# Performance work log

Measured on AMD Instinct MI355X. Metric: run time of the kernel, lower is better.

The kernel has to match this reference:

```python
import jax, jax.numpy as jnp
import numpy as np

D_K = 256

def setup_inputs() -> dict:
    key = jax.random.key(0)
    k1, k2, k3, k4 = jax.random.split(key, 4)
    B, S, D = 4, 4096, 256
    x = jax.random.normal(k1, (B, S, D), dtype=jnp.float32)
    scale = 1.0 / np.sqrt(D)
    W_q = jax.random.normal(k2, (D, D_K), dtype=jnp.float32) * scale
    W_k = jax.random.normal(k3, (D, D_K), dtype=jnp.float32) * scale
    W_v = jax.random.normal(k4, (D, D_K), dtype=jnp.float32) * scale
    return {"x": x, "W_q": W_q, "W_k": W_k, "W_v": W_v}

def reference(x, W_q, W_k, W_v):
    # x: [B, S, D]; weights: [D, d_k]
    B, S, D = x.shape
    Q = jnp.einsum('bsd,dk->bsk', x, W_q)
    K = jnp.einsum('bsd,dk->bsk', x, W_k)
    V = jnp.einsum('bsd,dk->bsk', x, W_v)
    scores = jnp.einsum('bqk,bsk->bqs', Q, K) / jnp.sqrt(jnp.float32(D_K))  # [B, S, S]
    causal = jnp.tril(jnp.ones((S, S), dtype=bool))
    scores = jnp.where(causal[None, :, :], scores, -jnp.inf)
    weights = jax.nn.softmax(scores, axis=-1)
    return jnp.einsum('bqs,bsk->bqk', weights, V)
```

## Files before the change

### kernel.cpp

```cpp
#include <hip/hip_runtime.h>
#include <hip/hip_bf16.h>
#include <cstdint>


typedef __bf16 b8v __attribute__((ext_vector_type(8)));
typedef __bf16 b4v __attribute__((ext_vector_type(4)));
typedef float  f4v __attribute__((ext_vector_type(4)));
typedef float  f16v __attribute__((ext_vector_type(16)));
typedef int    i4v __attribute__((ext_vector_type(4)));
typedef int    i2v __attribute__((ext_vector_type(2)));

#define MFMA16(a, b, c) __builtin_amdgcn_mfma_f32_16x16x32_bf16((a), (b), (c), 0, 0, 0)
#define MFMA32(a, b, c) __builtin_amdgcn_mfma_f32_32x32x16_bf16((a), (b), (c), 0, 0, 0)

#define GLOAD_LDS(gsrc, ldst)                                                        \
  __builtin_amdgcn_global_load_lds((const __attribute__((address_space(1))) void*)(gsrc), \
                                   (__attribute__((address_space(3))) void*)(ldst), 16, 0, 0)

#define SCALE_Q 0.09016844005f
#define MASKVAL -3.0e38f
#define M0VAL   -1.0e30f

static constexpr int UT = 4224;
static constexpr size_t WS_WT = 0;
static constexpr size_t WS_Q  = 524288;
static constexpr size_t WS_K  = WS_Q + 8388608;
static constexpr size_t WS_VT = WS_K + 8388608;
static constexpr size_t WS_PART = WS_VT + 8388608;

__global__ void prep_wt(const float* __restrict__ Wq, const float* __restrict__ Wk,
                        const float* __restrict__ Wv, __bf16* __restrict__ wt) {
  int gid = blockIdx.x * blockDim.x + threadIdx.x;
  int w = gid >> 16, rem = gid & 65535;
  int c = rem >> 8, d = rem & 255;
  const float* W = (w == 0) ? Wq : (w == 1) ? Wk : Wv;
  float v = W[d * 256 + c];
  if (w == 0) v *= SCALE_Q;
  wt[gid] = (__bf16)v;
}

__global__ void __launch_bounds__(256, 2) proj_qkv(
    const float* __restrict__ x, const __bf16* __restrict__ wt,
    __bf16* __restrict__ Qw, __bf16* __restrict__ Kw, __bf16* __restrict__ Vt) {
  __shared__ __bf16 w_lds[64][264];
  __shared__ __bf16 v_lds[64][72];
  const int tid = threadIdx.x;
  const int wv = tid >> 6, lane = tid & 63, c = lane & 15, g = lane >> 4;
  const int ww = blockIdx.x >> 8, rb = blockIdx.x & 255;
  const int rowbase = rb * 64;
  const int batch = rb >> 6, sblk = rb & 63;

  b8v xf[8];
  {
    const float* xr = x + (size_t)(rowbase + wv * 16 + c) * 256;
#pragma unroll
    for (int ks = 0; ks < 8; ++ks) {
      const float4 a0 = *reinterpret_cast<const float4*>(xr + 32 * ks + 8 * g);
      const float4 a1 = *reinterpret_cast<const float4*>(xr + 32 * ks + 8 * g + 4);
      b8v f;
      f[0] = (__bf16)a0.x; f[1] = (__bf16)a0.y; f[2] = (__bf16)a0.z; f[3] = (__bf16)a0.w;
      f[4] = (__bf16)a1.x; f[5] = (__bf16)a1.y; f[6] = (__bf16)a1.z; f[7] = (__bf16)a1.w;
      xf[ks] = f;
    }
  }
  const int srow = tid >> 2, sch = tid & 3;
  for (int ct = 0; ct < 4; ++ct) {
    __syncthreads();
    {
      const i4v* src = reinterpret_cast<const i4v*>(
          wt + ((size_t)(ww * 256 + ct * 64 + srow)) * 256 + sch * 64);
      i4v* dst = reinterpret_cast<i4v*>(&w_lds[srow][sch * 64]);
#pragma unroll
      for (int j = 0; j < 8; ++j) dst[j] = src[j];
    }
    __syncthreads();
    f4v pacc[4];
#pragma unroll
    for (int i = 0; i < 4; ++i) pacc[i] = (f4v){0.f, 0.f, 0.f, 0.f};
#pragma unroll
    for (int ks = 0; ks < 8; ++ks) {
#pragma unroll
      for (int nf = 0; nf < 4; ++nf) {
        b8v wf = *reinterpret_cast<const b8v*>(&w_lds[16 * nf + c][32 * ks + 8 * g]);
        pacc[nf] = MFMA16(xf[ks], wf, pacc[nf]);
      }
    }
    if (ww < 2) {
      __bf16* o = (ww == 0) ? Qw : Kw;
      const int row0 = rowbase + wv * 16 + 4 * g;
#pragma unroll
      for (int nf = 0; nf < 4; ++nf) {
        const int col = ct * 64 + 16 * nf + c;
#pragma unroll
        for (int r = 0; r < 4; ++r)
          o[(size_t)(row0 + r) * 256 + col] = (__bf16)pacc[nf][r];
      }
    } else {
      const int sp = 16 * wv + 4 * g;
#pragma unroll
      for (int nf = 0; nf < 4; ++nf) {
        b4v pk;
        pk[0] = (__bf16)pacc[nf][0]; pk[1] = (__bf16)pacc[nf][1];
        pk[2] = (__bf16)pacc[nf][2]; pk[3] = (__bf16)pacc[nf][3];
        *reinterpret_cast<b4v*>(&v_lds[16 * nf + c][sp]) = pk;
      }
      __syncthreads();
      {
        const int dd = tid >> 2, ch = tid & 3;
        const b8v* sp8 = reinterpret_cast<const b8v*>(&v_lds[dd][ch * 16]);
        __bf16* dst =
            Vt + ((size_t)(batch * 256 + ct * 64 + dd)) * 4096 + sblk * 64 + ch * 16;
        reinterpret_cast<b8v*>(dst)[0] = sp8[0];
        reinterpret_cast<b8v*>(dst)[1] = sp8[1];
      }
    }
  }
}

__global__ void __launch_bounds__(256, 2) attn_fwd(
    const __bf16* __restrict__ Qw, const __bf16* __restrict__ Kw,
    const __bf16* __restrict__ Vt, float* __restrict__ out,
    __bf16* __restrict__ part, float* __restrict__ ml, int NB) {
  extern __shared__ char smem[];
  float* bc = reinterpret_cast<float*>(smem + 65536);

  const int tid = threadIdx.x;
  const int wv = tid >> 6, lane = tid & 63;
  const int q5 = lane & 31, hi = lane >> 5;

  const int p = blockIdx.x, xcd = p & 7;
  const int lb = (xcd >> 1) * (NB >> 2) + (xcd & 1) * (NB >> 3) + (p >> 3);

  int u = (int)(((long long)lb * UT) / NB);
  const int u1 = (int)(((long long)(lb + 1) * UT) / NB);

  while (u < u1) {
    const int bb = u / 1056;
    const int r0 = u - bb * 1056;
    int q = 0;
    while ((q + 1) * (q + 2) <= r0) ++q;
    const int g0 = bb * 1056 + q * (q + 1);
    const int len = 2 * q + 2;
    const int ge = g0 + len;
    const int re = (u1 < ge) ? u1 : ge;
    const int ta = u - g0, tb = re - g0;
    const bool direct = (ta == 0) && (tb == len);

    const __bf16* Kg = Kw + (size_t)bb * 4096 * 256;
    const __bf16* Vg = Vt + (size_t)bb * 256 * 4096;

    auto stage = [&](int s, int tt) {
      char* Kd = smem + s * 32768;
      char* Vd = Kd + 16384;
#pragma unroll
      for (int i = 0; i < 4; ++i) {
        const int n = i * 256 + tid;
        const int r = n >> 5, cp = n & 31;
        const __bf16* src = Kg + (size_t)(tt * 32 + r) * 256 + ((cp ^ r) << 3);
        GLOAD_LDS(src, Kd + ((i * 256 + wv * 64) << 4));
      }
#pragma unroll
      for (int i = 0; i < 4; ++i) {
        const int n = i * 256 + tid;
        const int d = n >> 2, cp = n & 3;
        const __bf16* src =
            Vg + (size_t)d * 4096 + tt * 32 + ((cp ^ ((d >> 3) & 3)) << 3);
        GLOAD_LDS(src, Vd + ((i * 256 + wv * 64) << 4));
      }
    };

    b8v qf[16];
    {
      const __bf16* qr =
          Qw + ((size_t)(bb * 4096 + q * 128 + wv * 32 + q5)) * 256 + 8 * hi;
#pragma unroll
      for (int ks = 0; ks < 16; ++ks)
        qf[ks] = *reinterpret_cast<const b8v*>(qr + ks * 16);
    }

    f16v acc[8];
#pragma unroll
    for (int i = 0; i < 8; ++i)
#pragma unroll
      for (int j = 0; j < 16; ++j) acc[i][j] = 0.f;
    float m = M0VAL, lsum = 0.f;
    const int qg = q * 128 + wv * 32 + q5;
    const int ttEnd = 2 * tb;

    stage(0, 2 * ta);
    __syncthreads();

    for (int tt = 2 * ta; tt < ttEnd; ++tt) {
      const int cur = tt & 1;
      if (tt + 1 < ttEnd) stage(cur ^ 1, tt + 1);

      f16v s;
#pragma unroll
      for (int j = 0; j < 16; ++j) s[j] = 0.f;
      const char* kb0 = smem + cur * 32768 + q5 * 512;
      __builtin_amdgcn_s_setprio(1);
#pragma unroll
      for (int ks = 0; ks < 16; ++ks) {
        const int co = (((ks << 1) | hi) ^ q5) << 4;
        const b8v k0 = *reinterpret_cast<const b8v*>(kb0 + co);
        s = MFMA32(k0, qf[ks], s);
      }
      __builtin_amdgcn_s_setprio(0);

      if (tt * 32 + 31 > q * 128 + wv * 32) {
#pragma unroll
        for (int reg = 0; reg < 16; ++reg) {
          const int R = (reg & 3) + 8 * (reg >> 2) + 4 * hi;
          if (tt * 32 + R > qg) s[reg] = MASKVAL;
        }
      }
      float p0 = s[0], p1 = s[1], p2 = s[2], p3 = s[3];
#pragma unroll
      for (int j = 4; j < 16; j += 4) {
        p0 = fmaxf(p0, s[j]); p1 = fmaxf(p1, s[j + 1]);
        p2 = fmaxf(p2, s[j + 2]); p3 = fmaxf(p3, s[j + 3]);
      }
      const float pm = fmaxf(fmaxf(p0, p1), fmaxf(p2, p3));

      if (!__all(pm - m <= 8.0f)) {
        const float pm2 = fmaxf(pm, __shfl_xor(pm, 32));
        const float mnew = fmaxf(m, pm2);
        const float fac = exp2f(m - mnew);
        bc[wv * 32 + q5] = fac;
        lsum *= fac;
        m = mnew;
#pragma unroll
        for (int reg = 0; reg < 16; ++reg) {
          const float fr = bc[wv * 32 + ((reg & 3) + 8 * (reg >> 2) + 4 * hi)];
#pragma unroll
          for (int db = 0; db < 8; ++db) acc[db][reg] *= fr;
        }
      }
#pragma unroll
      for (int j = 0; j < 16; ++j) s[j] = exp2f(s[j] - m);
      {
        float u0 = 0.f, u1s = 0.f, u2 = 0.f, u3 = 0.f;
#pragma unroll
        for (int j = 0; j < 16; j += 4) {
          u0 += s[j]; u1s += s[j + 1]; u2 += s[j + 2]; u3 += s[j + 3];
        }
        lsum += (u0 + u1s) + (u2 + u3);
      }
      unsigned a0[4], a1[4];
#pragma unroll
      for (int mb = 0; mb < 4; ++mb) {
        b4v pk;
        pk[0] = (__bf16)s[4 * mb]; pk[1] = (__bf16)s[4 * mb + 1];
        pk[2] = (__bf16)s[4 * mb + 2]; pk[3] = (__bf16)s[4 * mb + 3];
        const uint2 uu = *reinterpret_cast<uint2*>(&pk);
        a0[mb] = uu.x; a1[mb] = uu.y;
      }
      const char* vbase = smem + cur * 32768 + 16384 + q5 * 64;
#pragma unroll
      for (int ks = 0; ks < 2; ++ks) {
        i4v wi;
#if __has_builtin(__builtin_amdgcn_permlane32_swap)
        const i2v e0 = __builtin_amdgcn_permlane32_swap((int)a0[2 * ks],
                                                        (int)a0[2 * ks + 1], false, false);
        const i2v e1 = __builtin_amdgcn_permlane32_swap((int)a1[2 * ks],
                                                        (int)a1[2 * ks + 1], false, false);
        wi[0] = e0[0]; wi[1] = e1[0]; wi[2] = e0[1]; wi[3] = e1[1];
#else
        const unsigned x0 = (unsigned)__shfl_xor((int)a0[2 * ks], 32);
        const unsigned x1 = (unsigned)__shfl_xor((int)a1[2 * ks], 32);
        const unsigned y0 = (unsigned)__shfl_xor((int)a0[2 * ks + 1], 32);
        const unsigned y1 = (unsigned)__shfl_xor((int)a1[2 * ks + 1], 32);
        wi[0] = hi ? (int)y0 : (int)a0[2 * ks];
        wi[1] = hi ? (int)y1 : (int)a1[2 * ks];
        wi[2] = hi ? (int)a0[2 * ks + 1] : (int)x0;
        wi[3] = hi ? (int)a1[2 * ks + 1] : (int)x1;
#endif
        const b8v pa = *reinterpret_cast<b8v*>(&wi);
        const int cov = ((((ks << 1) | hi)) ^ ((q5 >> 3) & 3)) << 4;
        __builtin_amdgcn_s_setprio(1);
#pragma unroll
        for (int db = 0; db < 8; ++db) {
          const b8v vf =
              *reinterpret_cast<const b8v*>(vbase + db * 2048 + cov);
          acc[db] = MFMA32(pa, vf, acc[db]);
        }
        __builtin_amdgcn_s_setprio(0);
      }
      __syncthreads();
    }

    lsum += __shfl_xor(lsum, 32);
    if (direct) {
      const float inv = 1.f / lsum;
      bc[wv * 32 + q5] = inv;
#pragma unroll
      for (int reg = 0; reg < 16; ++reg) {
        const int R = (reg & 3) + 8 * (reg >> 2) + 4 * hi;
        const float ivr = bc[wv * 32 + R];
        float* orow =
            out + ((size_t)(bb * 4096 + q * 128 + wv * 32 + R)) * 256 + q5;
#pragma unroll
        for (int db = 0; db < 8; ++db) orow[db * 32] = acc[db][reg] * ivr;
      }
    } else {
      const int sidx = bb * 32 + q;
      int base = 0;
      for (int sdx = 0; sdx < sidx; ++sdx) {
        const int sq = sdx & 31, sbb = sdx >> 5;
        const int h0 = sbb * 1056 + sq * (sq + 1);
        const int h1 = h0 + 2 * sq + 2;
        const int k = (h1 * NB + UT - 1) / UT - ((h0 + 1) * NB + UT - 1) / UT;
        if (k > 0) base += k + 1;
      }
      const int idx = ((u + 1) * NB + UT - 1) / UT - ((g0 + 1) * NB + UT - 1) / UT;
      const int slot = base + idx;
      __bf16* pbase = part + (size_t)slot * 32768;
#pragma unroll
      for (int reg = 0; reg < 16; ++reg) {
        const int R = (reg & 3) + 8 * (reg >> 2) + 4 * hi;
        __bf16* prow = pbase + (size_t)(wv * 32 + R) * 256 + q5;
#pragma unroll
        for (int db = 0; db < 8; ++db) prow[db * 32] = (__bf16)acc[db][reg];
      }
      if (hi == 0) {
        float2* ml2 = reinterpret_cast<float2*>(ml);
        ml2[(size_t)slot * 128 + wv * 32 + q5] = make_float2(m, lsum);
      }
    }
    u = re;
  }
}

__global__ void __launch_bounds__(256) combine_k(
    const __bf16* __restrict__ part, const float* __restrict__ ml,
    float* __restrict__ out, int NB) {
  const int sidx = blockIdx.x >> 2, rq = blockIdx.x & 3;
  const int bb = sidx >> 5, q = sidx & 31;
  const int g0 = bb * 1056 + q * (q + 1);
  const int g1 = g0 + 2 * q + 2;
  const int nbi = (g1 * NB + UT - 1) / UT - ((g0 + 1) * NB + UT - 1) / UT;
  if (nbi <= 0) return;
  const int nch = nbi + 1;
  int base = 0;
  for (int s = 0; s < sidx; ++s) {
    const int sq = s & 31, sbb = s >> 5;
    const int h0 = sbb * 1056 + sq * (sq + 1);
    const int h1 = h0 + 2 * sq + 2;
    const int k = (h1 * NB + UT - 1) / UT - ((h0 + 1) * NB + UT - 1) / UT;
    if (k > 0) base += k + 1;
  }
  const int row = rq * 32 + (threadIdx.x >> 3);
  const int c0 = (threadIdx.x & 7) * 32;
  const float2* ml2 = reinterpret_cast<const float2*>(ml);

  float mx = MASKVAL;
  for (int cc = 0; cc < nch; ++cc)
    mx = fmaxf(mx, ml2[(size_t)(base + cc) * 128 + row].x);
  float den = 0.f;
  for (int cc = 0; cc < nch; ++cc) {
    const float2 pr = ml2[(size_t)(base + cc) * 128 + row];
    den += exp2f(pr.x - mx) * pr.y;
  }
  const float inv = 1.f / den;
  f4v o4[8];
#pragma unroll
  for (int i = 0; i < 8; ++i) o4[i] = (f4v){0.f, 0.f, 0.f, 0.f};
  for (int cc = 0; cc < nch; ++cc) {
    const float w = exp2f(ml2[(size_t)(base + cc) * 128 + row].x - mx) * inv;
    const b8v* src = reinterpret_cast<const b8v*>(
        part + ((size_t)(base + cc) * 128 + row) * 256 + c0);
#pragma unroll
    for (int k = 0; k < 4; ++k) {
      const b8v v = src[k];
#pragma unroll
      for (int j = 0; j < 4; ++j) {
        o4[2 * k][j] += w * (float)v[j];
        o4[2 * k + 1][j] += w * (float)v[4 + j];
      }
    }
  }
  float* dst = out + ((size_t)(bb * 4096 + q * 128 + row)) * 256 + c0;
#pragma unroll
  for (int k = 0; k < 8; ++k) reinterpret_cast<f4v*>(dst)[k] = o4[k];
}

extern "C" void kernel_launch(void* const* d_in, const int* in_sizes, int n_in,
                              void* d_out, int out_size, void* d_ws, size_t ws_size,
                              hipStream_t stream) {
  const float* x  = reinterpret_cast<const float*>(d_in[0]);
  const float* Wq = reinterpret_cast<const float*>(d_in[1]);
  const float* Wk = reinterpret_cast<const float*>(d_in[2]);
  const float* Wv = reinterpret_cast<const float*>(d_in[3]);
  char* ws = reinterpret_cast<char*>(d_ws);
  __bf16* wt = reinterpret_cast<__bf16*>(ws + WS_WT);
  __bf16* Qw = reinterpret_cast<__bf16*>(ws + WS_Q);
  __bf16* Kw = reinterpret_cast<__bf16*>(ws + WS_K);
  __bf16* Vt = reinterpret_cast<__bf16*>(ws + WS_VT);
  float* out = reinterpret_cast<float*>(d_out);

  const int cand[5] = {512, 384, 256, 128, 64};
  int NB = 64, slots = 0;
  for (int ci = 0; ci < 5; ++ci) {
    const int nb = cand[ci];
    int sl = 0;
    for (int s = 0; s < 128; ++s) {
      const int sq = s & 31, sbb = s >> 5;
      const int h0 = sbb * 1056 + sq * (sq + 1);
      const int h1 = h0 + 2 * sq + 2;
      const int k = (h1 * nb + UT - 1) / UT - ((h0 + 1) * nb + UT - 1) / UT;
      if (k > 0) sl += k + 1;
    }
    const size_t need = WS_PART + (size_t)sl * 65536 + (size_t)sl * 1024;
    if (ws_size >= need) { NB = nb; slots = sl; break; }
  }
  __bf16* part = reinterpret_cast<__bf16*>(ws + WS_PART);
  float* mlp = reinterpret_cast<float*>(ws + WS_PART + (size_t)slots * 65536);

  prep_wt<<<768, 256, 0, stream>>>(Wq, Wk, Wv, wt);
  proj_qkv<<<768, 256, 0, stream>>>(x, wt, Qw, Kw, Vt);

  constexpr int kSmem = 66048;
  (void)hipFuncSetAttribute(reinterpret_cast<const void*>(attn_fwd),
                            hipFuncAttributeMaxDynamicSharedMemorySize, kSmem);
  attn_fwd<<<NB, 256, kSmem, stream>>>(Qw, Kw, Vt, out, part, mlp, NB);
  combine_k<<<512, 256, 0, stream>>>(part, mlp, out, NB);
}
```

Baseline: 162.6 us.

## Load K/V fragments directly from global memory instead of LDS double-buffering

Removes the LDS staging of K and V tiles (global_load_lds double buffer plus per-tile barriers). Each lane now reads its MFMA operands straight from global memory, relying on L2/L1 caching. The score MFMA chain is split into two independent accumulators to shorten the dependency chain. The LDS broadcasts of rescale factors are replaced with wave shuffles. This frees shared memory and barriers but makes all four waves re-fetch the same K/V data, and the V reads are strided with poor coalescing.

```diff
diff --git a/kernel.cpp b/kernel.cpp
--- a/kernel.cpp
+++ b/kernel.cpp
@@ -12,10 +12,6 @@
 
 #define MFMA16(a, b, c) __builtin_amdgcn_mfma_f32_16x16x32_bf16((a), (b), (c), 0, 0, 0)
 #define MFMA32(a, b, c) __builtin_amdgcn_mfma_f32_32x32x16_bf16((a), (b), (c), 0, 0, 0)
-
-#define GLOAD_LDS(gsrc, ldst)                                                        \
-  __builtin_amdgcn_global_load_lds((const __attribute__((address_space(1))) void*)(gsrc), \
-                                   (__attribute__((address_space(3))) void*)(ldst), 16, 0, 0)
 
 #define SCALE_Q 0.09016844005f
 #define MASKVAL -3.0e38f
@@ -121,9 +117,6 @@
     const __bf16* __restrict__ Qw, const __bf16* __restrict__ Kw,
     const __bf16* __restrict__ Vt, float* __restrict__ out,
     __bf16* __restrict__ part, float* __restrict__ ml, int NB) {
-  extern __shared__ char smem[];
-  float* bc = reinterpret_cast<float*>(smem + 65536);
-
   const int tid = threadIdx.x;
   const int wv = tid >> 6, lane = tid & 63;
   const int q5 = lane & 31, hi = lane >> 5;
@@ -146,28 +139,8 @@
     const int ta = u - g0, tb = re - g0;
     const bool direct = (ta == 0) && (tb == len);
 
-    const __bf16* Kg = Kw + (size_t)bb * 4096 * 256;
-    const __bf16* Vg = Vt + (size_t)bb * 256 * 4096;
-
-    auto stage = [&](int s, int tt) {
-      char* Kd = smem + s * 32768;
-      char* Vd = Kd + 16384;
-#pragma unroll
-      for (int i = 0; i < 4; ++i) {
-        const int n = i * 256 + tid;
-        const int r = n >> 5, cp = n & 31;
-        const __bf16* src = Kg + (size_t)(tt * 32 + r) * 256 + ((cp ^ r) << 3);
-        GLOAD_LDS(src, Kd + ((i * 256 + wv * 64) << 4));
-      }
-#pragma unroll
-      for (int i = 0; i < 4; ++i) {
-        const int n = i * 256 + tid;
-        const int d = n >> 2, cp = n & 3;
-        const __bf16* src =
-            Vg + (size_t)d * 4096 + tt * 32 + ((cp ^ ((d >> 3) & 3)) << 3);
-        GLOAD_LDS(src, Vd + ((i * 256 + wv * 64) << 4));
-      }
-    };
+    const __bf16* Krow = Kw + ((size_t)bb * 4096 + q5) * 256 + 8 * hi;
+    const __bf16* Vrow = Vt + ((size_t)bb * 256 + q5) * 4096 + 8 * hi;
 
     b8v qf[16];
     {
@@ -187,25 +160,21 @@
     const int qg = q * 128 + wv * 32 + q5;
     const int ttEnd = 2 * tb;
 
-    stage(0, 2 * ta);
-    __syncthreads();
-
     for (int tt = 2 * ta; tt < ttEnd; ++tt) {
-      const int cur = tt & 1;
-      if (tt + 1 < ttEnd) stage(cur ^ 1, tt + 1);
-
-      f16v s;
-#pragma unroll
-      for (int j = 0; j < 16; ++j) s[j] = 0.f;
-      const char* kb0 = smem + cur * 32768 + q5 * 512;
+      const __bf16* kbase = Krow + (size_t)tt * 32 * 256;
+      f16v sA, sB;
+#pragma unroll
+      for (int j = 0; j < 16; ++j) { sA[j] = 0.f; sB[j] = 0.f; }
       __builtin_amdgcn_s_setprio(1);
 #pragma unroll
-      for (int ks = 0; ks < 16; ++ks) {
-        const int co = (((ks << 1) | hi) ^ q5) << 4;
-        const b8v k0 = *reinterpret_cast<const b8v*>(kb0 + co);
-        s = MFMA32(k0, qf[ks], s);
+      for (int k8 = 0; k8 < 8; ++k8) {
+        const b8v ka = *reinterpret_cast<const b8v*>(kbase + k8 * 16);
+        const b8v kb = *reinterpret_cast<const b8v*>(kbase + 128 + k8 * 16);
+        sA = MFMA32(ka, qf[k8], sA);
+        sB = MFMA32(kb, qf[8 + k8], sB);
       }
       __builtin_amdgcn_s_setprio(0);
+      f16v s = sA + sB;
 
       if (tt * 32 + 31 > q * 128 + wv * 32) {
 #pragma unroll
@@ -226,12 +195,11 @@
         const float pm2 = fmaxf(pm, __shfl_xor(pm, 32));
         const float mnew = fmaxf(m, pm2);
         const float fac = exp2f(m - mnew);
-        bc[wv * 32 + q5] = fac;
         lsum *= fac;
         m = mnew;
 #pragma unroll
         for (int reg = 0; reg < 16; ++reg) {
-          const float fr = bc[wv * 32 + ((reg & 3) + 8 * (reg >> 2) + 4 * hi)];
+          const float fr = __shfl(fac, (reg & 3) + 8 * (reg >> 2) + 4 * hi);
 #pragma unroll
           for (int db = 0; db < 8; ++db) acc[db][reg] *= fr;
         }
@@ -255,7 +223,7 @@
         const uint2 uu = *reinterpret_cast<uint2*>(&pk);
         a0[mb] = uu.x; a1[mb] = uu.y;
       }
-      const char* vbase = smem + cur * 32768 + 16384 + q5 * 64;
+      const __bf16* vbase = Vrow + tt * 32;
 #pragma unroll
       for (int ks = 0; ks < 2; ++ks) {
         i4v wi;
@@ -276,27 +244,23 @@
         wi[3] = hi ? (int)a1[2 * ks + 1] : (int)x1;
 #endif
         const b8v pa = *reinterpret_cast<b8v*>(&wi);
-        const int cov = ((((ks << 1) | hi)) ^ ((q5 >> 3) & 3)) << 4;
         __builtin_amdgcn_s_setprio(1);
 #pragma unroll
         for (int db = 0; db < 8; ++db) {
-          const b8v vf =
-              *reinterpret_cast<const b8v*>(vbase + db * 2048 + cov);
+          const b8v vf = *reinterpret_cast<const b8v*>(vbase + (size_t)db * 131072 + ks * 16);
           acc[db] = MFMA32(pa, vf, acc[db]);
         }
         __builtin_amdgcn_s_setprio(0);
       }
-      __syncthreads();
     }
 
     lsum += __shfl_xor(lsum, 32);
     if (direct) {
       const float inv = 1.f / lsum;
-      bc[wv * 32 + q5] = inv;
 #pragma unroll
       for (int reg = 0; reg < 16; ++reg) {
         const int R = (reg & 3) + 8 * (reg >> 2) + 4 * hi;
-        const float ivr = bc[wv * 32 + R];
+        const float ivr = __shfl(inv, R);
         float* orow =
             out + ((size_t)(bb * 4096 + q * 128 + wv * 32 + R)) * 256 + q5;
 #pragma unroll
@@ -418,10 +382,6 @@
 
   prep_wt<<<768, 256, 0, stream>>>(Wq, Wk, Wv, wt);
   proj_qkv<<<768, 256, 0, stream>>>(x, wt, Qw, Kw, Vt);
-
-  constexpr int kSmem = 66048;
-  (void)hipFuncSetAttribute(reinterpret_cast<const void*>(attn_fwd),
-                            hipFuncAttributeMaxDynamicSharedMemorySize, kSmem);
-  attn_fwd<<<NB, 256, kSmem, stream>>>(Qw, Kw, Vt, out, part, mlp, NB);
+  attn_fwd<<<NB, 256, 0, stream>>>(Qw, Kw, Vt, out, part, mlp, NB);
   combine_k<<<512, 256, 0, stream>>>(part, mlp, out, NB);
 }
```

Result: slower. 222.7 us (+37.0%).

## Read V directly from global memory and split QK accumulation chains

Applied to the files above, without the earlier changes.

V tiles are no longer staged through LDS. Each lane reads its V fragments straight from global memory (mostly L2-resident), which halves LDS use to let more blocks fit per CU. The QK^T MFMA chain is also split into two independent accumulators to shorten the dependency chain. In exchange, every wave issues uncoalesced-ish global loads for V on the critical path of the PV MFMAs, with no prefetching.

```diff
diff --git a/kernel.cpp b/kernel.cpp
--- a/kernel.cpp
+++ b/kernel.cpp
@@ -122,7 +122,7 @@
     const __bf16* __restrict__ Vt, float* __restrict__ out,
     __bf16* __restrict__ part, float* __restrict__ ml, int NB) {
   extern __shared__ char smem[];
-  float* bc = reinterpret_cast<float*>(smem + 65536);
+  float* bc = reinterpret_cast<float*>(smem + 32768);
 
   const int tid = threadIdx.x;
   const int wv = tid >> 6, lane = tid & 63;
@@ -147,11 +147,10 @@
     const bool direct = (ta == 0) && (tb == len);
 
     const __bf16* Kg = Kw + (size_t)bb * 4096 * 256;
-    const __bf16* Vg = Vt + (size_t)bb * 256 * 4096;
+    const __bf16* Vrow = Vt + ((size_t)bb * 256 + q5) * 4096 + 8 * hi;
 
     auto stage = [&](int s, int tt) {
-      char* Kd = smem + s * 32768;
-      char* Vd = Kd + 16384;
+      char* Kd = smem + s * 16384;
 #pragma unroll
       for (int i = 0; i < 4; ++i) {
         const int n = i * 256 + tid;
@@ -159,14 +158,6 @@
         const __bf16* src = Kg + (size_t)(tt * 32 + r) * 256 + ((cp ^ r) << 3);
         GLOAD_LDS(src, Kd + ((i * 256 + wv * 64) << 4));
       }
-#pragma unroll
-      for (int i = 0; i < 4; ++i) {
-        const int n = i * 256 + tid;
-        const int d = n >> 2, cp = n & 3;
-        const __bf16* src =
-            Vg + (size_t)d * 4096 + tt * 32 + ((cp ^ ((d >> 3) & 3)) << 3);
-        GLOAD_LDS(src, Vd + ((i * 256 + wv * 64) << 4));
-      }
     };
 
     b8v qf[16];
@@ -194,18 +185,22 @@
       const int cur = tt & 1;
       if (tt + 1 < ttEnd) stage(cur ^ 1, tt + 1);
 
-      f16v s;
-#pragma unroll
-      for (int j = 0; j < 16; ++j) s[j] = 0.f;
-      const char* kb0 = smem + cur * 32768 + q5 * 512;
+      f16v sA, sB;
+#pragma unroll
+      for (int j = 0; j < 16; ++j) { sA[j] = 0.f; sB[j] = 0.f; }
+      const char* kb0 = smem + cur * 16384 + q5 * 512;
       __builtin_amdgcn_s_setprio(1);
 #pragma unroll
-      for (int ks = 0; ks < 16; ++ks) {
-        const int co = (((ks << 1) | hi) ^ q5) << 4;
-        const b8v k0 = *reinterpret_cast<const b8v*>(kb0 + co);
-        s = MFMA32(k0, qf[ks], s);
+      for (int k8 = 0; k8 < 8; ++k8) {
+        const int coA = (((k8 << 1) | hi) ^ q5) << 4;
+        const int coB = ((16 + (k8 << 1) | hi) ^ q5) << 4;
+        const b8v ka = *reinterpret_cast<const b8v*>(kb0 + coA);
+        const b8v kb = *reinterpret_cast<const b8v*>(kb0 + coB);
+        sA = MFMA32(ka, qf[k8], sA);
+        sB = MFMA32(kb, qf[8 + k8], sB);
       }
       __builtin_amdgcn_s_setprio(0);
+      f16v s = sA + sB;
 
       if (tt * 32 + 31 > q * 128 + wv * 32) {
 #pragma unroll
@@ -255,7 +250,7 @@
         const uint2 uu = *reinterpret_cast<uint2*>(&pk);
         a0[mb] = uu.x; a1[mb] = uu.y;
       }
-      const char* vbase = smem + cur * 32768 + 16384 + q5 * 64;
+      const __bf16* vbase = Vrow + tt * 32;
 #pragma unroll
       for (int ks = 0; ks < 2; ++ks) {
         i4v wi;
@@ -276,12 +271,11 @@
         wi[3] = hi ? (int)a1[2 * ks + 1] : (int)x1;
 #endif
         const b8v pa = *reinterpret_cast<b8v*>(&wi);
-        const int cov = ((((ks << 1) | hi)) ^ ((q5 >> 3) & 3)) << 4;
         __builtin_amdgcn_s_setprio(1);
 #pragma unroll
         for (int db = 0; db < 8; ++db) {
           const b8v vf =
-              *reinterpret_cast<const b8v*>(vbase + db * 2048 + cov);
+              *reinterpret_cast<const b8v*>(vbase + (size_t)db * 131072 + ks * 16);
           acc[db] = MFMA32(pa, vf, acc[db]);
         }
         __builtin_amdgcn_s_setprio(0);
@@ -419,7 +413,7 @@
   prep_wt<<<768, 256, 0, stream>>>(Wq, Wk, Wv, wt);
   proj_qkv<<<768, 256, 0, stream>>>(x, wt, Qw, Kw, Vt);
 
-  constexpr int kSmem = 66048;
+  constexpr int kSmem = 32768 + 1024;
   (void)hipFuncSetAttribute(reinterpret_cast<const void*>(attn_fwd),
                             hipFuncAttributeMaxDynamicSharedMemorySize, kSmem);
   attn_fwd<<<NB, 256, kSmem, stream>>>(Qw, Kw, Vt, out, part, mlp, NB);
```

Result: slower. 211.7 us (+30.2%).

## Write first split partial directly to output, split QK accumulator chains

Applied to the files above, without the earlier changes.

For split query blocks, the first chunk's unnormalized fp32 accumulator is now written straight into the output buffer, and only later chunks go to the bf16 partial buffer. The combine kernel reads that first chunk back from the output, so one bf16 partial slot per split block disappears and the workspace shrinks. The QK^T MFMA loop is split into two independent accumulator chains that are summed afterwards, to shorten the dependency chain between MFMAs. The NB=384 candidate is also dropped from the split-count search.

```diff
diff --git a/kernel.cpp b/kernel.cpp
--- a/kernel.cpp
+++ b/kernel.cpp
@@ -194,18 +194,22 @@
       const int cur = tt & 1;
       if (tt + 1 < ttEnd) stage(cur ^ 1, tt + 1);
 
-      f16v s;
-#pragma unroll
-      for (int j = 0; j < 16; ++j) s[j] = 0.f;
+      f16v sA, sB;
+#pragma unroll
+      for (int j = 0; j < 16; ++j) { sA[j] = 0.f; sB[j] = 0.f; }
       const char* kb0 = smem + cur * 32768 + q5 * 512;
       __builtin_amdgcn_s_setprio(1);
 #pragma unroll
-      for (int ks = 0; ks < 16; ++ks) {
-        const int co = (((ks << 1) | hi) ^ q5) << 4;
-        const b8v k0 = *reinterpret_cast<const b8v*>(kb0 + co);
-        s = MFMA32(k0, qf[ks], s);
+      for (int k8 = 0; k8 < 8; ++k8) {
+        const int cA = ((k8 << 1) | hi) ^ q5;
+        const int cB = ((16 + (k8 << 1)) | hi) ^ q5;
+        const b8v ka = *reinterpret_cast<const b8v*>(kb0 + (cA << 4));
+        const b8v kb = *reinterpret_cast<const b8v*>(kb0 + (cB << 4));
+        sA = MFMA32(ka, qf[k8], sA);
+        sB = MFMA32(kb, qf[8 + k8], sB);
       }
       __builtin_amdgcn_s_setprio(0);
+      f16v s = sA + sB;
 
       if (tt * 32 + 31 > q * 128 + wv * 32) {
 #pragma unroll
@@ -304,27 +308,37 @@
       }
     } else {
       const int sidx = bb * 32 + q;
-      int base = 0;
+      int base_p = 0, base_ml = 0;
       for (int sdx = 0; sdx < sidx; ++sdx) {
         const int sq = sdx & 31, sbb = sdx >> 5;
         const int h0 = sbb * 1056 + sq * (sq + 1);
         const int h1 = h0 + 2 * sq + 2;
         const int k = (h1 * NB + UT - 1) / UT - ((h0 + 1) * NB + UT - 1) / UT;
-        if (k > 0) base += k + 1;
+        if (k > 0) { base_p += k; base_ml += k + 1; }
       }
       const int idx = ((u + 1) * NB + UT - 1) / UT - ((g0 + 1) * NB + UT - 1) / UT;
-      const int slot = base + idx;
-      __bf16* pbase = part + (size_t)slot * 32768;
-#pragma unroll
-      for (int reg = 0; reg < 16; ++reg) {
-        const int R = (reg & 3) + 8 * (reg >> 2) + 4 * hi;
-        __bf16* prow = pbase + (size_t)(wv * 32 + R) * 256 + q5;
-#pragma unroll
-        for (int db = 0; db < 8; ++db) prow[db * 32] = (__bf16)acc[db][reg];
+      if (idx == 0) {
+#pragma unroll
+        for (int reg = 0; reg < 16; ++reg) {
+          const int R = (reg & 3) + 8 * (reg >> 2) + 4 * hi;
+          float* orow =
+              out + ((size_t)(bb * 4096 + q * 128 + wv * 32 + R)) * 256 + q5;
+#pragma unroll
+          for (int db = 0; db < 8; ++db) orow[db * 32] = acc[db][reg];
+        }
+      } else {
+        __bf16* pbase = part + (size_t)(base_p + idx - 1) * 32768;
+#pragma unroll
+        for (int reg = 0; reg < 16; ++reg) {
+          const int R = (reg & 3) + 8 * (reg >> 2) + 4 * hi;
+          __bf16* prow = pbase + (size_t)(wv * 32 + R) * 256 + q5;
+#pragma unroll
+          for (int db = 0; db < 8; ++db) prow[db * 32] = (__bf16)acc[db][reg];
+        }
       }
       if (hi == 0) {
         float2* ml2 = reinterpret_cast<float2*>(ml);
-        ml2[(size_t)slot * 128 + wv * 32 + q5] = make_float2(m, lsum);
+        ml2[(size_t)(base_ml + idx) * 128 + wv * 32 + q5] = make_float2(m, lsum);
       }
     }
     u = re;
@@ -340,35 +354,39 @@
   const int g1 = g0 + 2 * q + 2;
   const int nbi = (g1 * NB + UT - 1) / UT - ((g0 + 1) * NB + UT - 1) / UT;
   if (nbi <= 0) return;
-  const int nch = nbi + 1;
-  int base = 0;
+  int base_p = 0, base_ml = 0;
   for (int s = 0; s < sidx; ++s) {
     const int sq = s & 31, sbb = s >> 5;
     const int h0 = sbb * 1056 + sq * (sq + 1);
     const int h1 = h0 + 2 * sq + 2;
     const int k = (h1 * NB + UT - 1) / UT - ((h0 + 1) * NB + UT - 1) / UT;
-    if (k > 0) base += k + 1;
+    if (k > 0) { base_p += k; base_ml += k + 1; }
   }
   const int row = rq * 32 + (threadIdx.x >> 3);
   const int c0 = (threadIdx.x & 7) * 32;
   const float2* ml2 = reinterpret_cast<const float2*>(ml);
 
   float mx = MASKVAL;
-  for (int cc = 0; cc < nch; ++cc)
-    mx = fmaxf(mx, ml2[(size_t)(base + cc) * 128 + row].x);
+  for (int cc = 0; cc <= nbi; ++cc)
+    mx = fmaxf(mx, ml2[(size_t)(base_ml + cc) * 128 + row].x);
   float den = 0.f;
-  for (int cc = 0; cc < nch; ++cc) {
-    const float2 pr = ml2[(size_t)(base + cc) * 128 + row];
+  for (int cc = 0; cc <= nbi; ++cc) {
+    const float2 pr = ml2[(size_t)(base_ml + cc) * 128 + row];
     den += exp2f(pr.x - mx) * pr.y;
   }
   const float inv = 1.f / den;
+
+  float* dst = out + ((size_t)(bb * 4096 + q * 128 + row)) * 256 + c0;
   f4v o4[8];
-#pragma unroll
-  for (int i = 0; i < 8; ++i) o4[i] = (f4v){0.f, 0.f, 0.f, 0.f};
-  for (int cc = 0; cc < nch; ++cc) {
-    const float w = exp2f(ml2[(size_t)(base + cc) * 128 + row].x - mx) * inv;
+  {
+    const float w0 = exp2f(ml2[(size_t)base_ml * 128 + row].x - mx) * inv;
+#pragma unroll
+    for (int k = 0; k < 8; ++k) o4[k] = reinterpret_cast<const f4v*>(dst)[k] * w0;
+  }
+  for (int cc = 1; cc <= nbi; ++cc) {
+    const float w = exp2f(ml2[(size_t)(base_ml + cc) * 128 + row].x - mx) * inv;
     const b8v* src = reinterpret_cast<const b8v*>(
-        part + ((size_t)(base + cc) * 128 + row) * 256 + c0);
+        part + ((size_t)(base_p + cc - 1) * 128 + row) * 256 + c0);
 #pragma unroll
     for (int k = 0; k < 4; ++k) {
       const b8v v = src[k];
@@ -379,7 +397,6 @@
       }
     }
   }
-  float* dst = out + ((size_t)(bb * 4096 + q * 128 + row)) * 256 + c0;
 #pragma unroll
   for (int k = 0; k < 8; ++k) reinterpret_cast<f4v*>(dst)[k] = o4[k];
 }
@@ -398,23 +415,24 @@
   __bf16* Vt = reinterpret_cast<__bf16*>(ws + WS_VT);
   float* out = reinterpret_cast<float*>(d_out);
 
-  const int cand[5] = {512, 384, 256, 128, 64};
-  int NB = 64, slots = 0;
-  for (int ci = 0; ci < 5; ++ci) {
+  const int cand[4] = {512, 256, 128, 64};
+  int NB = 64;
+  size_t off_ml = 0;
+  for (int ci = 0; ci < 4; ++ci) {
     const int nb = cand[ci];
-    int sl = 0;
+    int sp = 0, sm = 0;
     for (int s = 0; s < 128; ++s) {
       const int sq = s & 31, sbb = s >> 5;
       const int h0 = sbb * 1056 + sq * (sq + 1);
       const int h1 = h0 + 2 * sq + 2;
       const int k = (h1 * nb + UT - 1) / UT - ((h0 + 1) * nb + UT - 1) / UT;
-      if (k > 0) sl += k + 1;
-    }
-    const size_t need = WS_PART + (size_t)sl * 65536 + (size_t)sl * 1024;
-    if (ws_size >= need) { NB = nb; slots = sl; break; }
+      if (k > 0) { sp += k; sm += k + 1; }
+    }
+    const size_t need = WS_PART + (size_t)sp * 65536 + (size_t)sm * 1024;
+    if (ws_size >= need) { NB = nb; off_ml = WS_PART + (size_t)sp * 65536; break; }
   }
   __bf16* part = reinterpret_cast<__bf16*>(ws + WS_PART);
-  float* mlp = reinterpret_cast<float*>(ws + WS_PART + (size_t)slots * 65536);
+  float* mlp = reinterpret_cast<float*>(ws + off_ml);
 
   prep_wt<<<768, 256, 0, stream>>>(Wq, Wk, Wv, wt);
   proj_qkv<<<768, 256, 0, stream>>>(x, wt, Qw, Kw, Vt);
```

New measurement: 207.1 us. 27.4% more time.
